# Optimization experiments

Measured on AMD Instinct MI355X. Metric: run time of the kernel, lower is better.

The kernel has to match this reference:

```python
import jax, jax.numpy as jnp
import numpy as np

MARGIN = 1.0
EPS = 1e-6  # torch F.pairwise_distance eps used inside TripletMarginLoss


def _cdist(x):
    # Euclidean pairwise distance via gram matrix (avoids [N,N,D] intermediate)
    sq = jnp.sum(x * x, axis=1)  # [N]
    d2 = sq[:, None] + sq[None, :] - 2.0 * (x @ x.T)
    return jnp.sqrt(jnp.maximum(d2, 0.0))


def setup_inputs() -> dict:
    key = jax.random.key(0)
    k1, k2 = jax.random.split(key)
    embeddings = jax.random.normal(k1, (4096, 512), dtype=jnp.float32)
    labels = jax.random.randint(k2, (4096,), 0, 16, dtype=jnp.int64)
    return {"embeddings": embeddings, "labels": labels}


def reference(embeddings, labels):
    n = embeddings.shape[0]
    pd = _cdist(embeddings)  # [N, N]
    same = labels[:, None] == labels[None, :]
    eye = jnp.eye(n, dtype=bool)
    pos_mask = same & ~eye          # same label, not self
    neg_mask = ~same                # different label

    # hardest positive: max distance among positives; hardest negative: min among negatives
    pos_idx = jnp.argmax(jnp.where(pos_mask, pd, -jnp.inf), axis=1)  # [N]
    neg_idx = jnp.argmin(jnp.where(neg_mask, pd, jnp.inf), axis=1)   # [N]
    valid = pos_mask.any(axis=1) & neg_mask.any(axis=1)              # [N] bool

    a = embeddings
    p = embeddings[pos_idx]
    ng = embeddings[neg_idx]
    # torch TripletMarginLoss: ||a - p + eps||_2, ||a - n + eps||_2
    d_ap = jnp.sqrt(jnp.sum((a - p + EPS) ** 2, axis=1))
    d_an = jnp.sqrt(jnp.sum((a - ng + EPS) ** 2, axis=1))
    per = jnp.maximum(d_ap - d_an + MARGIN, 0.0)
    cnt = jnp.sum(valid)
    loss = jnp.sum(jnp.where(valid, per, 0.0)) / jnp.maximum(cnt, 1)
    return loss
```

## Files before the change

### kernel.cpp

```cpp
#include <hip/hip_runtime.h>
#include <math.h>

#define N 4096
#define D 512
#define NS2 64
#define NT 48

typedef __attribute__((ext_vector_type(8))) short short8;
typedef __attribute__((ext_vector_type(8))) unsigned short ushort8;
typedef __attribute__((ext_vector_type(4))) float f32x4;

static __device__ __forceinline__ unsigned short f2bf(float f) {
    unsigned u = __float_as_uint(f);
    u = (u + 0x7fffu + ((u >> 16) & 1u)) >> 16;
    return (unsigned short)u;
}
static __device__ __forceinline__ float bf2f(unsigned short b) {
    return __uint_as_float(((unsigned)b) << 16);
}

__global__ __launch_bounds__(256) void k_split_sq(const float* __restrict__ X,
                                                  unsigned short* __restrict__ Xhi,
                                                  unsigned short* __restrict__ Xlo,
                                                  float* __restrict__ sq) {
    const int wave = threadIdx.x >> 6;
    const int lane = threadIdx.x & 63;
    const int row = blockIdx.x * 4 + wave;
    const float* xr = X + (size_t)row * D + lane * 8;
    float4 v0 = *(const float4*)(xr);
    float4 v1 = *(const float4*)(xr + 4);
    float v[8] = {v0.x, v0.y, v0.z, v0.w, v1.x, v1.y, v1.z, v1.w};
    ushort8 hv, lv;
    float s = 0.f;
#pragma unroll
    for (int j = 0; j < 8; ++j) {
        float f = v[j];
        unsigned short hb = f2bf(f);
        float hf = bf2f(hb);
        unsigned short lb = f2bf(f - hf);
        hv[j] = hb;
        lv[j] = lb;
        s += f * f;
    }
    *(ushort8*)(Xhi + (size_t)row * D + lane * 8) = hv;
    *(ushort8*)(Xlo + (size_t)row * D + lane * 8) = lv;
#pragma unroll
    for (int off = 32; off >= 1; off >>= 1) s += __shfl_xor(s, off);
    if (lane == 0) sq[row] = s;
}

__global__ __launch_bounds__(256) void k_tile_mfma(
    const unsigned short* __restrict__ Xhi, const unsigned short* __restrict__ Xlo,
    const int* __restrict__ labels, const float* __restrict__ sq,
    float* __restrict__ pmaxv, int* __restrict__ pmaxi,
    float* __restrict__ pminv, int* __restrict__ pmini) {
    __shared__ unsigned short As[128 * 32];
    __shared__ unsigned short Bs[128 * 32];
    __shared__ float sqr[128], sqc[128];
    __shared__ int labr[128], labc[128];

    const int ct = blockIdx.x, rt = blockIdx.y;
    const int row0 = rt * 128, col0 = ct * 128;
    const int tid = threadIdx.x;
    const int w = tid >> 6, lane = tid & 63;
    const int wr = w >> 1, wc = w & 1;
    const int g = lane >> 4, c = lane & 15;

    if (tid < 128) {
        sqr[tid] = sq[row0 + tid];
        labr[tid] = labels[row0 + tid];
    } else {
        int t = tid - 128;
        sqc[t] = sq[col0 + t];
        labc[t] = labels[col0 + t];
    }

    f32x4 acc[4][4];
#pragma unroll
    for (int i = 0; i < 4; ++i)
#pragma unroll
        for (int j = 0; j < 4; ++j) acc[i][j] = (f32x4){0.f, 0.f, 0.f, 0.f};

    const int srow = lane >> 2;
    const int scol = (lane & 3) * 8;

    const unsigned short* Aterm[3] = {Xhi, Xhi, Xlo};
    const unsigned short* Bterm[3] = {Xhi, Xlo, Xhi};

    for (int s = 0; s < NT; ++s) {
        const int t = s >> 4;
        const int k0 = (s & 15) * 32;
        const unsigned short* Ap = Aterm[t];
        const unsigned short* Bp = Bterm[t];
#pragma unroll
        for (int i = 0; i < 2; ++i) {
            const int r = (w * 2 + i) * 16 + srow;
            __builtin_amdgcn_global_load_lds(
                (const __attribute__((address_space(1))) unsigned int*)(Ap + (size_t)(row0 + r) * D + k0 + scol),
                (__attribute__((address_space(3))) unsigned int*)&As[(w * 2 + i) * 512],
                16, 0, 0);
            __builtin_amdgcn_global_load_lds(
                (const __attribute__((address_space(1))) unsigned int*)(Bp + (size_t)(col0 + r) * D + k0 + scol),
                (__attribute__((address_space(3))) unsigned int*)&Bs[(w * 2 + i) * 512],
                16, 0, 0);
        }
        __syncthreads();

        short8 af[4], bf[4];
#pragma unroll
        for (int i = 0; i < 4; ++i) {
            af[i] = *(const short8*)&As[(wr * 64 + i * 16 + c) * 32 + g * 8];
            bf[i] = *(const short8*)&Bs[(wc * 64 + i * 16 + c) * 32 + g * 8];
        }
#pragma unroll
        for (int i = 0; i < 4; ++i)
#pragma unroll
            for (int j = 0; j < 4; ++j)
                acc[i][j] = __builtin_amdgcn_mfma_f32_16x16x32_bf16(af[i], bf[j], acc[i][j], 0, 0, 0);
        __syncthreads();
    }

    const int cs = ct * 2 + wc;
#pragma unroll
    for (int i = 0; i < 4; ++i) {
#pragma unroll
        for (int q = 0; q < 4; ++q) {
            const int rloc = wr * 64 + i * 16 + g * 4 + q;
            const int r = row0 + rloc;
            const int lr = labr[rloc];
            const float sr = sqr[rloc];
            float pv = -INFINITY, nv = INFINITY;
            int pi = 0x7fffffff, ni = 0x7fffffff;
#pragma unroll
            for (int j = 0; j < 4; ++j) {
                const int cloc = wc * 64 + j * 16 + c;
                const int cg = col0 + cloc;
                float d2 = sr + sqc[cloc] - 2.f * acc[i][j][q];
                float pd = sqrtf(fmaxf(d2, 0.f));
                if (cg == r) continue;
                if (lr == labc[cloc]) {
                    if (pd > pv || (pd == pv && cg < pi)) { pv = pd; pi = cg; }
                } else {
                    if (pd < nv || (pd == nv && cg < ni)) { nv = pd; ni = cg; }
                }
            }
#pragma unroll
            for (int st = 1; st < 16; st <<= 1) {
                float ov = __shfl_xor(pv, st);
                int oi = __shfl_xor(pi, st);
                if (ov > pv || (ov == pv && oi < pi)) { pv = ov; pi = oi; }
                float ov2 = __shfl_xor(nv, st);
                int oi2 = __shfl_xor(ni, st);
                if (ov2 < nv || (ov2 == nv && oi2 < ni)) { nv = ov2; ni = oi2; }
            }
            if (c == 0) {
                pmaxv[(size_t)r * NS2 + cs] = pv;
                pmaxi[(size_t)r * NS2 + cs] = pi;
                pminv[(size_t)r * NS2 + cs] = nv;
                pmini[(size_t)r * NS2 + cs] = ni;
            }
        }
    }
}

__global__ __launch_bounds__(256) void k_final(
    const float* __restrict__ X,
    const float* __restrict__ pmaxv, const int* __restrict__ pmaxi,
    const float* __restrict__ pminv, const int* __restrict__ pmini,
    float* __restrict__ bsum, int* __restrict__ bcnt) {
    __shared__ float ssum[4];
    __shared__ int scnt[4];
    const int wave = threadIdx.x >> 6, lane = threadIdx.x & 63;
    const int row = blockIdx.x * 4 + wave;

    float pv = pmaxv[(size_t)row * NS2 + lane];
    int pi = pmaxi[(size_t)row * NS2 + lane];
    float nv = pminv[(size_t)row * NS2 + lane];
    int ni = pmini[(size_t)row * NS2 + lane];
#pragma unroll
    for (int s = 1; s < 64; s <<= 1) {
        float ov = __shfl_xor(pv, s);
        int oi = __shfl_xor(pi, s);
        if (ov > pv || (ov == pv && oi < pi)) { pv = ov; pi = oi; }
        float ov2 = __shfl_xor(nv, s);
        int oi2 = __shfl_xor(ni, s);
        if (ov2 < nv || (ov2 == nv && oi2 < ni)) { nv = ov2; ni = oi2; }
    }
    const bool valid = (pv != -INFINITY) && (nv != INFINITY);
    const int pidx = (pi == 0x7fffffff) ? 0 : pi;
    const int nidx = (ni == 0x7fffffff) ? 0 : ni;

    const float* xa = X + (size_t)row * D + lane * 8;
    const float* xp = X + (size_t)pidx * D + lane * 8;
    const float* xn = X + (size_t)nidx * D + lane * 8;
    float4 a0 = *(const float4*)(xa), a1 = *(const float4*)(xa + 4);
    float4 p0 = *(const float4*)(xp), p1 = *(const float4*)(xp + 4);
    float4 n0 = *(const float4*)(xn), n1 = *(const float4*)(xn + 4);
    float sap = 0.f, san = 0.f;
    {
        float d;
        d = a0.x - p0.x + 1e-6f; sap += d * d;
        d = a0.y - p0.y + 1e-6f; sap += d * d;
        d = a0.z - p0.z + 1e-6f; sap += d * d;
        d = a0.w - p0.w + 1e-6f; sap += d * d;
        d = a1.x - p1.x + 1e-6f; sap += d * d;
        d = a1.y - p1.y + 1e-6f; sap += d * d;
        d = a1.z - p1.z + 1e-6f; sap += d * d;
        d = a1.w - p1.w + 1e-6f; sap += d * d;
        d = a0.x - n0.x + 1e-6f; san += d * d;
        d = a0.y - n0.y + 1e-6f; san += d * d;
        d = a0.z - n0.z + 1e-6f; san += d * d;
        d = a0.w - n0.w + 1e-6f; san += d * d;
        d = a1.x - n1.x + 1e-6f; san += d * d;
        d = a1.y - n1.y + 1e-6f; san += d * d;
        d = a1.z - n1.z + 1e-6f; san += d * d;
        d = a1.w - n1.w + 1e-6f; san += d * d;
    }
#pragma unroll
    for (int off = 32; off >= 1; off >>= 1) {
        sap += __shfl_xor(sap, off);
        san += __shfl_xor(san, off);
    }
    if (lane == 0) {
        float d_ap = sqrtf(sap), d_an = sqrtf(san);
        float per = valid ? fmaxf(d_ap - d_an + 1.0f, 0.f) : 0.f;
        ssum[wave] = per;
        scnt[wave] = valid ? 1 : 0;
    }
    __syncthreads();
    if (threadIdx.x == 0) {
        bsum[blockIdx.x] = ssum[0] + ssum[1] + ssum[2] + ssum[3];
        bcnt[blockIdx.x] = scnt[0] + scnt[1] + scnt[2] + scnt[3];
    }
}

__global__ __launch_bounds__(256) void k_out(const float* __restrict__ bsum,
                                             const int* __restrict__ bcnt,
                                             float* __restrict__ out) {
    __shared__ float ss[256];
    __shared__ int sc[256];
    const int t = threadIdx.x;
    float s = 0.f;
    int c = 0;
    for (int i = t; i < N / 4; i += 256) {
        s += bsum[i];
        c += bcnt[i];
    }
    ss[t] = s;
    sc[t] = c;
    __syncthreads();
    for (int off = 128; off >= 1; off >>= 1) {
        if (t < off) {
            ss[t] += ss[t + off];
            sc[t] += sc[t + off];
        }
        __syncthreads();
    }
    if (t == 0) out[0] = ss[0] / (float)max(sc[0], 1);
}

extern "C" void kernel_launch(void* const* d_in, const int* in_sizes, int n_in,
                              void* d_out, int out_size, void* d_ws, size_t ws_size,
                              hipStream_t stream) {
    const float* X = (const float*)d_in[0];
    const int* labels = (const int*)d_in[1];

    float* sq = (float*)d_ws;
    unsigned short* Xhi = (unsigned short*)(sq + N);
    unsigned short* Xlo = Xhi + (size_t)N * D;
    float* pmaxv = (float*)(Xlo + (size_t)N * D);
    float* pminv = pmaxv + (size_t)N * NS2;
    int* pmaxi = (int*)(pminv + (size_t)N * NS2);
    int* pmini = pmaxi + (size_t)N * NS2;
    float* bsum = (float*)(pmini + (size_t)N * NS2);
    int* bcnt = (int*)(bsum + N / 4);
    float* out = (float*)d_out;

    k_split_sq<<<N / 4, 256, 0, stream>>>(X, Xhi, Xlo, sq);
    k_tile_mfma<<<dim3(N / 128, N / 128), 256, 0, stream>>>(Xhi, Xlo, labels, sq,
                                                            pmaxv, pmaxi, pminv, pmini);
    k_final<<<N / 4, 256, 0, stream>>>(X, pmaxv, pmaxi, pminv, pmini, bsum, bcnt);
    k_out<<<1, 256, 0, stream>>>(bsum, bcnt, out);
}
```

Baseline: 178.8 us.

## Exploit distance-matrix symmetry with upper-triangular tiles and fuse final reduction

```diff
diff --git a/kernel.cpp b/kernel.cpp
--- a/kernel.cpp
+++ b/kernel.cpp
@@ -4,7 +4,7 @@
 #define N 4096
 #define D 512
 #define NS2 64
-#define NT 48
+#define NBLK 1024
 
 typedef __attribute__((ext_vector_type(8))) short short8;
 typedef __attribute__((ext_vector_type(8))) unsigned short ushort8;
@@ -22,7 +22,9 @@
 __global__ __launch_bounds__(256) void k_split_sq(const float* __restrict__ X,
                                                   unsigned short* __restrict__ Xhi,
                                                   unsigned short* __restrict__ Xlo,
-                                                  float* __restrict__ sq) {
+                                                  float* __restrict__ sq,
+                                                  int* __restrict__ counter) {
+    if (blockIdx.x == 0 && threadIdx.x == 0) counter[0] = 0;
     const int wave = threadIdx.x >> 6;
     const int lane = threadIdx.x & 63;
     const int row = blockIdx.x * 4 + wave;
@@ -59,7 +61,11 @@
     __shared__ float sqr[128], sqc[128];
     __shared__ int labr[128], labc[128];
 
-    const int ct = blockIdx.x, rt = blockIdx.y;
+    int rem = blockIdx.x;
+    int rt = 0;
+    while (rem >= (32 - rt)) { rem -= (32 - rt); ++rt; }
+    const int ct = rt + rem;
+
     const int row0 = rt * 128, col0 = ct * 128;
     const int tid = threadIdx.x;
     const int w = tid >> 6, lane = tid & 63;
@@ -81,46 +87,43 @@
 #pragma unroll
         for (int j = 0; j < 4; ++j) acc[i][j] = (f32x4){0.f, 0.f, 0.f, 0.f};
 
-    const int srow = lane >> 2;
-    const int scol = (lane & 3) * 8;
-
-    const unsigned short* Aterm[3] = {Xhi, Xhi, Xlo};
-    const unsigned short* Bterm[3] = {Xhi, Xlo, Xhi};
-
-    for (int s = 0; s < NT; ++s) {
-        const int t = s >> 4;
-        const int k0 = (s & 15) * 32;
-        const unsigned short* Ap = Aterm[t];
-        const unsigned short* Bp = Bterm[t];
-#pragma unroll
-        for (int i = 0; i < 2; ++i) {
-            const int r = (w * 2 + i) * 16 + srow;
-            __builtin_amdgcn_global_load_lds(
-                (const __attribute__((address_space(1))) unsigned int*)(Ap + (size_t)(row0 + r) * D + k0 + scol),
-                (__attribute__((address_space(3))) unsigned int*)&As[(w * 2 + i) * 512],
-                16, 0, 0);
-            __builtin_amdgcn_global_load_lds(
-                (const __attribute__((address_space(1))) unsigned int*)(Bp + (size_t)(col0 + r) * D + k0 + scol),
-                (__attribute__((address_space(3))) unsigned int*)&Bs[(w * 2 + i) * 512],
-                16, 0, 0);
+#pragma unroll
+    for (int t = 0; t < 3; ++t) {
+        const unsigned short* Ap = (t == 2) ? Xlo : Xhi;
+        const unsigned short* Bp = (t == 1) ? Xlo : Xhi;
+        for (int ks = 0; ks < 16; ++ks) {
+            const int k0 = ks * 32;
+            const int srow = lane >> 2;
+            const int scol = (lane & 3) * 8;
+#pragma unroll
+            for (int i = 0; i < 2; ++i) {
+                const int r = (w * 2 + i) * 16 + srow;
+                __builtin_amdgcn_global_load_lds(
+                    (const __attribute__((address_space(1))) unsigned int*)(Ap + (size_t)(row0 + r) * D + k0 + scol),
+                    (__attribute__((address_space(3))) unsigned int*)&As[(w * 2 + i) * 512],
+                    16, 0, 0);
+                __builtin_amdgcn_global_load_lds(
+                    (const __attribute__((address_space(1))) unsigned int*)(Bp + (size_t)(col0 + r) * D + k0 + scol),
+                    (__attribute__((address_space(3))) unsigned int*)&Bs[(w * 2 + i) * 512],
+                    16, 0, 0);
+            }
+            __syncthreads();
+
+            short8 af[4], bf[4];
+#pragma unroll
+            for (int i = 0; i < 4; ++i) {
+                af[i] = *(const short8*)&As[(wr * 64 + i * 16 + c) * 32 + g * 8];
+                bf[i] = *(const short8*)&Bs[(wc * 64 + i * 16 + c) * 32 + g * 8];
+            }
+#pragma unroll
+            for (int i = 0; i < 4; ++i)
+#pragma unroll
+                for (int j = 0; j < 4; ++j)
+                    acc[i][j] = __builtin_amdgcn_mfma_f32_16x16x32_bf16(af[i], bf[j], acc[i][j], 0, 0, 0);
+            __syncthreads();
         }
-        __syncthreads();
-
-        short8 af[4], bf[4];
-#pragma unroll
-        for (int i = 0; i < 4; ++i) {
-            af[i] = *(const short8*)&As[(wr * 64 + i * 16 + c) * 32 + g * 8];
-            bf[i] = *(const short8*)&Bs[(wc * 64 + i * 16 + c) * 32 + g * 8];
-        }
-#pragma unroll
-        for (int i = 0; i < 4; ++i)
-#pragma unroll
-            for (int j = 0; j < 4; ++j)
-                acc[i][j] = __builtin_amdgcn_mfma_f32_16x16x32_bf16(af[i], bf[j], acc[i][j], 0, 0, 0);
-        __syncthreads();
-    }
-
-    const int cs = ct * 2 + wc;
+    }
+
 #pragma unroll
     for (int i = 0; i < 4; ++i) {
 #pragma unroll
@@ -154,10 +157,54 @@
                 if (ov2 < nv || (ov2 == nv && oi2 < ni)) { nv = ov2; ni = oi2; }
             }
             if (c == 0) {
-                pmaxv[(size_t)r * NS2 + cs] = pv;
-                pmaxi[(size_t)r * NS2 + cs] = pi;
-                pminv[(size_t)r * NS2 + cs] = nv;
-                pmini[(size_t)r * NS2 + cs] = ni;
+                const int slot = ct * 2 + wc;
+                pmaxv[(size_t)r * NS2 + slot] = pv;
+                pmaxi[(size_t)r * NS2 + slot] = pi;
+                pminv[(size_t)r * NS2 + slot] = nv;
+                pmini[(size_t)r * NS2 + slot] = ni;
+            }
+        }
+    }
+
+    if (rt != ct) {
+#pragma unroll
+        for (int j = 0; j < 4; ++j) {
+            const int cloc = wc * 64 + j * 16 + c;
+            const int cg = col0 + cloc;
+            const int lcol = labc[cloc];
+            const float scv = sqc[cloc];
+            float pv = -INFINITY, nv = INFINITY;
+            int pi = 0x7fffffff, ni = 0x7fffffff;
+#pragma unroll
+            for (int i = 0; i < 4; ++i) {
+#pragma unroll
+                for (int q = 0; q < 4; ++q) {
+                    const int rloc = wr * 64 + i * 16 + g * 4 + q;
+                    const int rg = row0 + rloc;
+                    float d2 = scv + sqr[rloc] - 2.f * acc[i][j][q];
+                    float pd = sqrtf(fmaxf(d2, 0.f));
+                    if (lcol == labr[rloc]) {
+                        if (pd > pv || (pd == pv && rg < pi)) { pv = pd; pi = rg; }
+                    } else {
+                        if (pd < nv || (pd == nv && rg < ni)) { nv = pd; ni = rg; }
+                    }
+                }
+            }
+#pragma unroll
+            for (int st = 16; st < 64; st <<= 1) {
+                float ov = __shfl_xor(pv, st);
+                int oi = __shfl_xor(pi, st);
+                if (ov > pv || (ov == pv && oi < pi)) { pv = ov; pi = oi; }
+                float ov2 = __shfl_xor(nv, st);
+                int oi2 = __shfl_xor(ni, st);
+                if (ov2 < nv || (ov2 == nv && oi2 < ni)) { nv = ov2; ni = oi2; }
+            }
+            if (g == 0) {
+                const int slot = rt * 2 + wr;
+                pmaxv[(size_t)cg * NS2 + slot] = pv;
+                pmaxi[(size_t)cg * NS2 + slot] = pi;
+                pminv[(size_t)cg * NS2 + slot] = nv;
+                pmini[(size_t)cg * NS2 + slot] = ni;
             }
         }
     }
@@ -167,7 +214,8 @@
     const float* __restrict__ X,
     const float* __restrict__ pmaxv, const int* __restrict__ pmaxi,
     const float* __restrict__ pminv, const int* __restrict__ pmini,
-    float* __restrict__ bsum, int* __restrict__ bcnt) {
+    float* __restrict__ bsum, int* __restrict__ bcnt,
+    int* __restrict__ counter, float* __restrict__ out) {
     __shared__ float ssum[4];
     __shared__ int scnt[4];
     const int wave = threadIdx.x >> 6, lane = threadIdx.x & 63;
@@ -228,35 +276,40 @@
         scnt[wave] = valid ? 1 : 0;
     }
     __syncthreads();
+    __shared__ int isLast;
     if (threadIdx.x == 0) {
-        bsum[blockIdx.x] = ssum[0] + ssum[1] + ssum[2] + ssum[3];
-        bcnt[blockIdx.x] = scnt[0] + scnt[1] + scnt[2] + scnt[3];
-    }
-}
-
-__global__ __launch_bounds__(256) void k_out(const float* __restrict__ bsum,
-                                             const int* __restrict__ bcnt,
-                                             float* __restrict__ out) {
-    __shared__ float ss[256];
-    __shared__ int sc[256];
+        float bs = ssum[0] + ssum[1] + ssum[2] + ssum[3];
+        int bc = scnt[0] + scnt[1] + scnt[2] + scnt[3];
+        __hip_atomic_store(&bsum[blockIdx.x], bs, __ATOMIC_RELAXED, __HIP_MEMORY_SCOPE_AGENT);
+        __hip_atomic_store(&bcnt[blockIdx.x], bc, __ATOMIC_RELAXED, __HIP_MEMORY_SCOPE_AGENT);
+        __threadfence();
+        int prev = __hip_atomic_fetch_add(counter, 1, __ATOMIC_ACQ_REL, __HIP_MEMORY_SCOPE_AGENT);
+        isLast = (prev == (int)gridDim.x - 1);
+    }
+    __syncthreads();
+    if (!isLast) return;
+
+    __threadfence();
+    __shared__ float rs[256];
+    __shared__ int rc[256];
     const int t = threadIdx.x;
     float s = 0.f;
-    int c = 0;
-    for (int i = t; i < N / 4; i += 256) {
-        s += bsum[i];
-        c += bcnt[i];
-    }
-    ss[t] = s;
-    sc[t] = c;
+    int cc = 0;
+    for (int i = t; i < NBLK; i += 256) {
+        s += __hip_atomic_load(&bsum[i], __ATOMIC_RELAXED, __HIP_MEMORY_SCOPE_AGENT);
+        cc += __hip_atomic_load(&bcnt[i], __ATOMIC_RELAXED, __HIP_MEMORY_SCOPE_AGENT);
+    }
+    rs[t] = s;
+    rc[t] = cc;
     __syncthreads();
     for (int off = 128; off >= 1; off >>= 1) {
         if (t < off) {
-            ss[t] += ss[t + off];
-            sc[t] += sc[t + off];
+            rs[t] += rs[t + off];
+            rc[t] += rc[t + off];
         }
         __syncthreads();
     }
-    if (t == 0) out[0] = ss[0] / (float)max(sc[0], 1);
+    if (t == 0) out[0] = rs[0] / (float)max(rc[0], 1);
 }
 
 extern "C" void kernel_launch(void* const* d_in, const int* in_sizes, int n_in,
@@ -273,12 +326,11 @@
     int* pmaxi = (int*)(pminv + (size_t)N * NS2);
     int* pmini = pmaxi + (size_t)N * NS2;
     float* bsum = (float*)(pmini + (size_t)N * NS2);
-    int* bcnt = (int*)(bsum + N / 4);
+    int* bcnt = (int*)(bsum + NBLK);
+    int* counter = bcnt + NBLK;
     float* out = (float*)d_out;
 
-    k_split_sq<<<N / 4, 256, 0, stream>>>(X, Xhi, Xlo, sq);
-    k_tile_mfma<<<dim3(N / 128, N / 128), 256, 0, stream>>>(Xhi, Xlo, labels, sq,
-                                                            pmaxv, pmaxi, pminv, pmini);
-    k_final<<<N / 4, 256, 0, stream>>>(X, pmaxv, pmaxi, pminv, pmini, bsum, bcnt);
-    k_out<<<1, 256, 0, stream>>>(bsum, bcnt, out);
-}
+    k_split_sq<<<N / 4, 256, 0, stream>>>(X, Xhi, Xlo, sq, counter);
+    k_tile_mfma<<<528, 256, 0, stream>>>(Xhi, Xlo, labels, sq, pmaxv, pmaxi, pminv, pmini);
+    k_final<<<NBLK, 256, 0, stream>>>(X, pmaxv, pmaxi, pminv, pmini, bsum, bcnt, counter, out);
+}
```

After: 245.4 us. 1.37x slower.
